# Kernel tuning notes

Measured on AMD Instinct MI355X. Metric: run time of the kernel, lower is better.

## Reference

```python
import jax, jax.numpy as jnp
import numpy as np
from jax.scipy.special import logsumexp

EPSILON = 0.05
MAX_ITER = 50
TOL = 0.001


def setup_inputs() -> dict:
    key = jax.random.key(0)
    k1, k2, k3 = jax.random.split(key, 3)
    B, N, M = 32, 1024, 1024
    cost = jax.random.uniform(k1, (B, N, M), dtype=jnp.float32)  # non-negative
    src = jax.random.uniform(k2, (B, N), dtype=jnp.float32) + 0.1
    tgt = jax.random.uniform(k3, (B, M), dtype=jnp.float32) + 0.1
    src = src / jnp.sum(src, axis=-1, keepdims=True)
    tgt = tgt / jnp.sum(tgt, axis=-1, keepdims=True)
    return {"cost": cost, "source_marginal": src, "target_marginal": tgt}


def reference(cost, source_marginal, target_marginal):
    B, N, M = cost.shape
    log_r = jnp.log(source_marginal + 1e-12)  # [B,N]
    log_c = jnp.log(target_marginal + 1e-12)  # [B,M]
    log_K = -cost / EPSILON                    # [B,N,M]

    log_u0 = jnp.zeros((B, N), dtype=cost.dtype)
    log_v0 = jnp.zeros((B, M), dtype=cost.dtype)

    def step(carry, _):
        log_u, log_v, done = carry
        # row update: logsumexp over M
        new_u = log_r - logsumexp(log_K + log_v[:, None, :], axis=-1)
        # col update: logsumexp over N (uses freshly updated u, as in torch)
        new_v = log_c - logsumexp(log_K + new_u[:, :, None], axis=-2)
        change = jnp.max(jnp.abs(new_u - log_u))  # global max, like torch
        # emulate early break: freeze state once converged
        log_u_next = jnp.where(done, log_u, new_u)
        log_v_next = jnp.where(done, log_v, new_v)
        done_next = done | (change < TOL)
        return (log_u_next, log_v_next, done_next), None

    (log_u, log_v, _), _ = jax.lax.scan(
        step, (log_u0, log_v0, jnp.array(False)), None, length=MAX_ITER
    )

    log_T = log_u[:, :, None] + log_K + log_v[:, None, :]
    return jnp.exp(log_T)
```

## Files before the change

### kernel.cpp

```cpp
#include <hip/hip_runtime.h>
#include <math.h>

#define INV_EPS  (-20.0f)
#define QINV     (1.0f / 65535.0f)
#define LN65535  11.090354888959125f
#define TOLV     0.001f
#define MAX_ITER 50
#define NBLK     256
#define NTHR     1024

#define CTRL_CNT(g)   ((g) * 64)
#define CTRL_GEN(g)   ((g) * 64 + 32)
#define CTRL_ARR(d)   (2048 + (d) * 32)
#define CTRL_CHG(d)   (3648 + (d) * 32)
#define CTRL_INTS     5248
#define Q_OFF_BYTES   (1u << 20)

#define RX __ATOMIC_RELAXED
#define SC __HIP_MEMORY_SCOPE_AGENT

__device__ __forceinline__ float wave_red_sum64(float x) {
    x += __int_as_float(__builtin_amdgcn_update_dpp(0, __float_as_int(x), 0x111, 0xf, 0xf, false));
    x += __int_as_float(__builtin_amdgcn_update_dpp(0, __float_as_int(x), 0x112, 0xf, 0xf, false));
    x += __int_as_float(__builtin_amdgcn_update_dpp(0, __float_as_int(x), 0x114, 0xf, 0xf, false));
    x += __int_as_float(__builtin_amdgcn_update_dpp(0, __float_as_int(x), 0x118, 0xf, 0xf, false));
    x += __int_as_float(__builtin_amdgcn_update_dpp(0, __float_as_int(x), 0x142, 0xf, 0xf, false));
    x += __int_as_float(__builtin_amdgcn_update_dpp(0, __float_as_int(x), 0x143, 0xf, 0xf, false));
    return __int_as_float(__builtin_amdgcn_readlane(__float_as_int(x), 63));
}

__device__ __forceinline__ void group_sync(int* cnt, int* gen) {
    __syncthreads();
    if (threadIdx.x == 0) {
        int g = __hip_atomic_load(gen, RX, SC);
        int a = __hip_atomic_fetch_add(cnt, 1, RX, SC);
        if (a == 7) {
            __hip_atomic_store(cnt, 0, RX, SC);
            __hip_atomic_store(gen, g + 1, RX, SC);
        } else {
            while (__hip_atomic_load(gen, RX, SC) == g)
                __builtin_amdgcn_s_sleep(1);
        }
    }
    __syncthreads();
}

#define ROWMATH(LR)                                                            \
  {                                                                            \
    float sA = fmaf(qf0, evs0, fmaf(qf4, evs4, fmaf(qf8,  evs8,  qf12*evs12)));\
    float sB = fmaf(qf1, evs1, fmaf(qf5, evs5, fmaf(qf9,  evs9,  qf13*evs13)));\
    float sC = fmaf(qf2, evs2, fmaf(qf6, evs6, fmaf(qf10, evs10, qf14*evs14)));\
    float sD = fmaf(qf3, evs3, fmaf(qf7, evs7, fmaf(qf11, evs11, qf15*evs15)));\
    float s = (sA + sB) + (sC + sD);                                           \
    s = wave_red_sum64(s);                                                     \
    float u_new = lg_src[LR] - __logf(s);                                      \
    flag |= (fabsf(u_new - u_ring[pv][LR]) >= TOLV);                           \
    if (lane == 0) u_ring[cur][LR] = u_new;                                    \
    float eu = __expf(u_new);                                                  \
    cs0 = fmaf(qf0, eu, cs0);   cs1 = fmaf(qf1, eu, cs1);                      \
    cs2 = fmaf(qf2, eu, cs2);   cs3 = fmaf(qf3, eu, cs3);                      \
    cs4 = fmaf(qf4, eu, cs4);   cs5 = fmaf(qf5, eu, cs5);                      \
    cs6 = fmaf(qf6, eu, cs6);   cs7 = fmaf(qf7, eu, cs7);                      \
    cs8 = fmaf(qf8, eu, cs8);   cs9 = fmaf(qf9, eu, cs9);                      \
    cs10 = fmaf(qf10, eu, cs10); cs11 = fmaf(qf11, eu, cs11);                  \
    cs12 = fmaf(qf12, eu, cs12); cs13 = fmaf(qf13, eu, cs13);                  \
    cs14 = fmaf(qf14, eu, cs14); cs15 = fmaf(qf15, eu, cs15);                  \
  }

#define ROW_LIN(QA, QB, LR)                                                    \
  {                                                                            \
    float qf0  = (float)((QA).x & 0xffffu), qf1  = (float)((QA).x >> 16),      \
          qf2  = (float)((QA).y & 0xffffu), qf3  = (float)((QA).y >> 16),      \
          qf4  = (float)((QA).z & 0xffffu), qf5  = (float)((QA).z >> 16),      \
          qf6  = (float)((QA).w & 0xffffu), qf7  = (float)((QA).w >> 16),      \
          qf8  = (float)((QB).x & 0xffffu), qf9  = (float)((QB).x >> 16),      \
          qf10 = (float)((QB).y & 0xffffu), qf11 = (float)((QB).y >> 16),      \
          qf12 = (float)((QB).z & 0xffffu), qf13 = (float)((QB).z >> 16),      \
          qf14 = (float)((QB).w & 0xffffu), qf15 = (float)((QB).w >> 16);      \
    ROWMATH(LR)                                                                \
  }

template<int QM>
__global__ __launch_bounds__(NTHR, 4) void sinkhorn_fused(
    const float* __restrict__ cost, const float* __restrict__ src,
    const float* __restrict__ tgt, float* __restrict__ out,
    int* __restrict__ ctrl, uint* __restrict__ qbuf)
{
    const int t    = threadIdx.x;
    const int lane = t & 63;
    const int widx = t >> 6;
    const int rx   = blockIdx.x & 7;
    const int sx   = blockIdx.x >> 3;
    const int grp  = rx * 4 + (sx >> 3);
    const int j    = sx & 7;

    __shared__ float smS[16][64][17];
    __shared__ float v_ring[4][1024];
    __shared__ float u_ring[4][128];
    __shared__ float lg_tgt[1024];
    __shared__ float lg_src[128];
    __shared__ int   s_chg, s_stop;

    int* cnt = ctrl + CTRL_CNT(grp);
    int* gen = ctrl + CTRL_GEN(grp);

    const int rowb = (grp << 10) + (j << 7);
    const float* cbase = cost + ((size_t)(rowb + (widx << 3)) << 10) + (lane << 2);
    uint4* qb4 = nullptr;
    if constexpr (QM == 1)
        qb4 = (uint4*)qbuf + (size_t)(rowb + (widx << 3)) * 128 + lane;
    float* const Pg = out + ((size_t)grp << 20);

    lg_tgt[t] = __logf(tgt[(grp << 10) + t] + 1e-12f) + ((QM == 1) ? LN65535 : 0.f);
    if (t < 128) {
        lg_src[t]    = __logf(src[rowb + t] + 1e-12f);
        u_ring[3][t] = 0.f;
    }
    v_ring[3][t] = 0.f;

    float4 f0, f1, f2, f3, g0, g1, g2, g3;
    if constexpr (QM == 0) {
        f0 = *(const float4*)(cbase);
        f1 = *(const float4*)(cbase + 256);
        f2 = *(const float4*)(cbase + 512);
        f3 = *(const float4*)(cbase + 768);
        const float* r1p = cbase + ((size_t)1 << 10);
        g0 = *(const float4*)(r1p);
        g1 = *(const float4*)(r1p + 256);
        g2 = *(const float4*)(r1p + 512);
        g3 = *(const float4*)(r1p + 768);
    }
    uint4 uf0 = {}, uf1 = {}, ug0 = {}, ug1 = {};

    __syncthreads();

    int K = -1;
    for (int it = 0; it < MAX_ITER; ++it) {
        const int cur = it & 3, pv = (it + 3) & 3;

        if (t == 0) {
            int stop = 0;
            if (it >= 2) {
                const int d = it - 2;
                while (__hip_atomic_load(ctrl + CTRL_ARR(d), RX, SC) != NBLK)
                    __builtin_amdgcn_s_sleep(1);
                stop = (__hip_atomic_load(ctrl + CTRL_CHG(d), RX, SC) == 0);
            }
            s_stop = stop;
            s_chg  = 0;
        }
        __syncthreads();
        if (s_stop) { K = it - 2; break; }

        bool flag = false;

        if constexpr (QM == 1) {
            const int r8 = widx << 3;
            const float* vp = &v_ring[pv][lane << 2];
            float4 va = *(const float4*)vp;
            float4 vb = *(const float4*)(vp + 256);
            float4 vc = *(const float4*)(vp + 512);
            float4 vd = *(const float4*)(vp + 768);
            const float evs0  = __expf(va.x)*QINV, evs1  = __expf(va.y)*QINV,
                        evs2  = __expf(va.z)*QINV, evs3  = __expf(va.w)*QINV,
                        evs4  = __expf(vb.x)*QINV, evs5  = __expf(vb.y)*QINV,
                        evs6  = __expf(vb.z)*QINV, evs7  = __expf(vb.w)*QINV,
                        evs8  = __expf(vc.x)*QINV, evs9  = __expf(vc.y)*QINV,
                        evs10 = __expf(vc.z)*QINV, evs11 = __expf(vc.w)*QINV,
                        evs12 = __expf(vd.x)*QINV, evs13 = __expf(vd.y)*QINV,
                        evs14 = __expf(vd.z)*QINV, evs15 = __expf(vd.w)*QINV;
            float cs0=0,cs1=0,cs2=0,cs3=0,cs4=0,cs5=0,cs6=0,cs7=0,
                  cs8=0,cs9=0,cs10=0,cs11=0,cs12=0,cs13=0,cs14=0,cs15=0;

            if (it == 0) {
                float4 a0 = *(const float4*)(cbase);
                float4 a1 = *(const float4*)(cbase + 256);
                float4 a2 = *(const float4*)(cbase + 512);
                float4 a3 = *(const float4*)(cbase + 768);
                const float* r1p = cbase + ((size_t)1 << 10);
                float4 b0 = *(const float4*)(r1p);
                float4 b1 = *(const float4*)(r1p + 256);
                float4 b2 = *(const float4*)(r1p + 512);
                float4 b3 = *(const float4*)(r1p + 768);
                #pragma unroll 1
                for (int i = 0; i < 8; ++i) {
                    const float* nxt = cbase + ((size_t)((i + 2) & 7) << 10);
                    float4 p0 = *(const float4*)(nxt);
                    float4 p1 = *(const float4*)(nxt + 256);
                    float4 p2 = *(const float4*)(nxt + 512);
                    float4 p3 = *(const float4*)(nxt + 768);

                    float qf0  = rintf(__expf(a0.x*INV_EPS)*65535.f);
                    float qf1  = rintf(__expf(a0.y*INV_EPS)*65535.f);
                    float qf2  = rintf(__expf(a0.z*INV_EPS)*65535.f);
                    float qf3  = rintf(__expf(a0.w*INV_EPS)*65535.f);
                    float qf4  = rintf(__expf(a1.x*INV_EPS)*65535.f);
                    float qf5  = rintf(__expf(a1.y*INV_EPS)*65535.f);
                    float qf6  = rintf(__expf(a1.z*INV_EPS)*65535.f);
                    float qf7  = rintf(__expf(a1.w*INV_EPS)*65535.f);
                    float qf8  = rintf(__expf(a2.x*INV_EPS)*65535.f);
                    float qf9  = rintf(__expf(a2.y*INV_EPS)*65535.f);
                    float qf10 = rintf(__expf(a2.z*INV_EPS)*65535.f);
                    float qf11 = rintf(__expf(a2.w*INV_EPS)*65535.f);
                    float qf12 = rintf(__expf(a3.x*INV_EPS)*65535.f);
                    float qf13 = rintf(__expf(a3.y*INV_EPS)*65535.f);
                    float qf14 = rintf(__expf(a3.z*INV_EPS)*65535.f);
                    float qf15 = rintf(__expf(a3.w*INV_EPS)*65535.f);
                    uint4 w0, w1;
                    w0.x = (uint)qf0  | ((uint)qf1  << 16);
                    w0.y = (uint)qf2  | ((uint)qf3  << 16);
                    w0.z = (uint)qf4  | ((uint)qf5  << 16);
                    w0.w = (uint)qf6  | ((uint)qf7  << 16);
                    w1.x = (uint)qf8  | ((uint)qf9  << 16);
                    w1.y = (uint)qf10 | ((uint)qf11 << 16);
                    w1.z = (uint)qf12 | ((uint)qf13 << 16);
                    w1.w = (uint)qf14 | ((uint)qf15 << 16);
                    qb4[(i << 7)]      = w0;
                    qb4[(i << 7) + 64] = w1;

                    ROWMATH(r8 + i)

                    a0 = b0; a1 = b1; a2 = b2; a3 = b3;
                    b0 = p0; b1 = p1; b2 = p2; b3 = p3;
                }
            } else {
                #pragma unroll 1
                for (int i = 0; i < 8; ++i) {
                    const int nx = ((i + 2) & 7) << 7;
                    uint4 up0 = qb4[nx];
                    uint4 up1 = qb4[nx + 64];
                    ROW_LIN(uf0, uf1, r8 + i)
                    uf0 = ug0; uf1 = ug1; ug0 = up0; ug1 = up1;
                }
            }

            smS[widx][lane][0]  = cs0;  smS[widx][lane][1]  = cs1;
            smS[widx][lane][2]  = cs2;  smS[widx][lane][3]  = cs3;
            smS[widx][lane][4]  = cs4;  smS[widx][lane][5]  = cs5;
            smS[widx][lane][6]  = cs6;  smS[widx][lane][7]  = cs7;
            smS[widx][lane][8]  = cs8;  smS[widx][lane][9]  = cs9;
            smS[widx][lane][10] = cs10; smS[widx][lane][11] = cs11;
            smS[widx][lane][12] = cs12; smS[widx][lane][13] = cs13;
            smS[widx][lane][14] = cs14; smS[widx][lane][15] = cs15;
        } else {
            const float* vp = &v_ring[pv][lane << 2];
            float4 vo0 = *(const float4*)(vp);
            float4 vo1 = *(const float4*)(vp + 256);
            float4 vo2 = *(const float4*)(vp + 512);
            float4 vo3 = *(const float4*)(vp + 768);
            float cs[16];
            #pragma unroll
            for (int s = 0; s < 16; ++s) cs[s] = 0.f;
            #pragma unroll 1
            for (int i = 0; i < 8; ++i) {
                const float* nxt = cbase + ((size_t)((i + 2) & 7) << 10);
                float4 p0 = *(const float4*)(nxt);
                float4 p1 = *(const float4*)(nxt + 256);
                float4 p2 = *(const float4*)(nxt + 512);
                float4 p3 = *(const float4*)(nxt + 768);
                float e[16];
                e[ 0] = __expf(fmaf(f0.x, INV_EPS, vo0.x));
                e[ 1] = __expf(fmaf(f0.y, INV_EPS, vo0.y));
                e[ 2] = __expf(fmaf(f0.z, INV_EPS, vo0.z));
                e[ 3] = __expf(fmaf(f0.w, INV_EPS, vo0.w));
                e[ 4] = __expf(fmaf(f1.x, INV_EPS, vo1.x));
                e[ 5] = __expf(fmaf(f1.y, INV_EPS, vo1.y));
                e[ 6] = __expf(fmaf(f1.z, INV_EPS, vo1.z));
                e[ 7] = __expf(fmaf(f1.w, INV_EPS, vo1.w));
                e[ 8] = __expf(fmaf(f2.x, INV_EPS, vo2.x));
                e[ 9] = __expf(fmaf(f2.y, INV_EPS, vo2.y));
                e[10] = __expf(fmaf(f2.z, INV_EPS, vo2.z));
                e[11] = __expf(fmaf(f2.w, INV_EPS, vo2.w));
                e[12] = __expf(fmaf(f3.x, INV_EPS, vo3.x));
                e[13] = __expf(fmaf(f3.y, INV_EPS, vo3.y));
                e[14] = __expf(fmaf(f3.z, INV_EPS, vo3.z));
                e[15] = __expf(fmaf(f3.w, INV_EPS, vo3.w));
                float s01 = e[0]+e[1],   s23 = e[2]+e[3];
                float s45 = e[4]+e[5],   s67 = e[6]+e[7];
                float s89 = e[8]+e[9],   sab = e[10]+e[11];
                float scd = e[12]+e[13], sef = e[14]+e[15];
                float s = ((s01+s23)+(s45+s67)) + ((s89+sab)+(scd+sef));
                s = wave_red_sum64(s);
                const int lr = (widx << 3) + i;
                float u_new = lg_src[lr] - __logf(s);
                flag |= (fabsf(u_new - u_ring[pv][lr]) >= TOLV);
                if (lane == 0) u_ring[cur][lr] = u_new;
                float eu = __expf(u_new);
                #pragma unroll
                for (int k = 0; k < 16; ++k)
                    cs[k] = fmaf(e[k], eu, cs[k]);
                f0 = g0; f1 = g1; f2 = g2; f3 = g3;
                g0 = p0; g1 = p1; g2 = p2; g3 = p3;
            }
            #pragma unroll
            for (int s = 0; s < 16; ++s) smS[widx][lane][s] = cs[s];
        }

        if (lane == 0 && flag) s_chg = 1;
        __syncthreads();

        if (QM == 1 && it == 0) {
            uf0 = qb4[0];   uf1 = qb4[64];
            ug0 = qb4[128]; ug1 = qb4[192];
        }

        if (t == 0) {
            if (s_chg)
                __hip_atomic_fetch_or(ctrl + CTRL_CHG(it), 1, RX, SC);
            asm volatile("s_waitcnt vmcnt(0)" ::: "memory");
            __hip_atomic_fetch_add(ctrl + CTRL_ARR(it), 1, RX, SC);
        }

        float* Pb = Pg + (size_t)(((it & 1) << 3) + j) * 1040;
        {
            const int L  = (t >> 2) & 63;
            const int sl = ((t >> 8) << 2) | (t & 3);
            float S = 0.f;
            #pragma unroll
            for (int w = 0; w < 16; ++w) S += smS[w][L][sl];
            if constexpr (QM == 0) S *= __expf(-v_ring[pv][t]);
            __hip_atomic_store(Pb + t, S, RX, SC);
        }

        group_sync(cnt, gen);

        {
            float* Pf = Pg + (size_t)((it & 1) << 3) * 1040;
            float S = 0.f;
            #pragma unroll
            for (int jj = 0; jj < 8; ++jj)
                S += __hip_atomic_load(Pf + jj * 1040 + t, RX, SC);
            v_ring[cur][t] = lg_tgt[t] - __logf(S);
        }
        __syncthreads();
    }

    if (K < 0) {
        if (t == 0) {
            while (__hip_atomic_load(ctrl + CTRL_ARR(48), RX, SC) != NBLK)
                __builtin_amdgcn_s_sleep(1);
            s_stop = (__hip_atomic_load(ctrl + CTRL_CHG(48), RX, SC) == 0);
        }
        __syncthreads();
        K = s_stop ? 48 : 49;
    }

    group_sync(cnt, gen);

    {
        const int slot = K & 3;
        const size_t base = ((size_t)rowb) << 10;
        if constexpr (QM == 1) {
            lg_tgt[t] = __expf(v_ring[slot][t]) * QINV;
            __syncthreads();
            const uint2* q2 = (const uint2*)qbuf;
            #pragma unroll 1
            for (int i = 0; i < 32; ++i) {
                const int g4  = (i << 10) + t;
                const int lr  = g4 >> 8;
                const int m0  = (g4 & 255) << 2;
                const int c   = m0 >> 8;
                const int ln  = (m0 >> 2) & 63;
                const size_t u4i = (size_t)(((rowb + lr) << 1) + (c >> 1)) * 64 + ln;
                uint2 w = q2[(u4i << 1) + (c & 1)];
                float4 ev4 = *(const float4*)&lg_tgt[m0];
                const float uu = __expf(u_ring[slot][lr]);
                float4 o;
                o.x = (float)(w.x & 0xffffu) * (uu * ev4.x);
                o.y = (float)(w.x >> 16)     * (uu * ev4.y);
                o.z = (float)(w.y & 0xffffu) * (uu * ev4.z);
                o.w = (float)(w.y >> 16)     * (uu * ev4.w);
                *(float4*)(out + base + ((size_t)g4 << 2)) = o;
            }
        } else {
            #pragma unroll 1
            for (int i = 0; i < 32; ++i) {
                const int g4  = (i << 10) + t;
                const int lr  = g4 >> 8;
                const int c4  = (g4 & 255) << 2;
                const size_t e = base + ((size_t)g4 << 2);
                float4 cc = *(const float4*)(cost + e);
                float4 vv = *(const float4*)&v_ring[slot][c4];
                const float uu = u_ring[slot][lr];
                float4 o;
                o.x = __expf(fmaf(cc.x, INV_EPS, uu + vv.x));
                o.y = __expf(fmaf(cc.y, INV_EPS, uu + vv.y));
                o.z = __expf(fmaf(cc.z, INV_EPS, uu + vv.z));
                o.w = __expf(fmaf(cc.w, INV_EPS, uu + vv.w));
                *(float4*)(out + e) = o;
            }
        }
    }
}

extern "C" void kernel_launch(void* const* d_in, const int* in_sizes, int n_in,
                              void* d_out, int out_size, void* d_ws, size_t ws_size,
                              hipStream_t stream) {
    const float* cost = (const float*)d_in[0];
    const float* src  = (const float*)d_in[1];
    const float* tgt  = (const float*)d_in[2];
    float* out = (float*)d_out;
    int*   ctrl = (int*)d_ws;
    (void)in_sizes; (void)n_in; (void)out_size;

    hipMemsetAsync(d_ws, 0, CTRL_INTS * sizeof(int), stream);

    const size_t need = (size_t)Q_OFF_BYTES + ((size_t)64 << 20);
    if (ws_size >= need) {
        uint* qbuf = (uint*)((char*)d_ws + Q_OFF_BYTES);
        sinkhorn_fused<1><<<dim3(NBLK), dim3(NTHR), 0, stream>>>(
            cost, src, tgt, out, ctrl, qbuf);
    } else {
        sinkhorn_fused<0><<<dim3(NBLK), dim3(NTHR), 0, stream>>>(
            cost, src, tgt, out, ctrl, nullptr);
    }
}
```

Baseline: 309.6 us.

## Stash half of quantized kernel in LDS and use LDS atomics for column sums

```diff
diff --git a/kernel.cpp b/kernel.cpp
--- a/kernel.cpp
+++ b/kernel.cpp
@@ -80,6 +80,48 @@
     ROWMATH(LR)                                                                \
   }
 
+#define COL_ATOMIC                                                             \
+  { const int lb = (lane << 2) + (lane >> 2);                                  \
+    atomicAdd(&colAcc[lb      ], cs0);  atomicAdd(&colAcc[lb +   1], cs1);     \
+    atomicAdd(&colAcc[lb +   2], cs2);  atomicAdd(&colAcc[lb +   3], cs3);     \
+    atomicAdd(&colAcc[lb + 272], cs4);  atomicAdd(&colAcc[lb + 273], cs5);     \
+    atomicAdd(&colAcc[lb + 274], cs6);  atomicAdd(&colAcc[lb + 275], cs7);     \
+    atomicAdd(&colAcc[lb + 544], cs8);  atomicAdd(&colAcc[lb + 545], cs9);     \
+    atomicAdd(&colAcc[lb + 546], cs10); atomicAdd(&colAcc[lb + 547], cs11);    \
+    atomicAdd(&colAcc[lb + 816], cs12); atomicAdd(&colAcc[lb + 817], cs13);    \
+    atomicAdd(&colAcc[lb + 818], cs14); atomicAdd(&colAcc[lb + 819], cs15); }
+
+#define LQS(r, p) (((((widx << 2) | (r)) << 1) | (p)) * 64 + lane)
+
+#define EPI_ROW(QA, QB, i)                                                     \
+  { const float uu = __expf(u_ring[slot][(widx << 3) + (i)]);                  \
+    float* op = out + (((size_t)(rowb + (widx << 3) + (i))) << 10) + (lane << 2); \
+    float4 ev, o;                                                              \
+    ev = *(const float4*)&lg_tgt[lane << 2];                                   \
+    o.x = (float)((QA).x & 0xffffu) * (uu * ev.x);                             \
+    o.y = (float)((QA).x >> 16)     * (uu * ev.y);                             \
+    o.z = (float)((QA).y & 0xffffu) * (uu * ev.z);                             \
+    o.w = (float)((QA).y >> 16)     * (uu * ev.w);                             \
+    *(float4*)(op) = o;                                                        \
+    ev = *(const float4*)&lg_tgt[256 + (lane << 2)];                           \
+    o.x = (float)((QA).z & 0xffffu) * (uu * ev.x);                             \
+    o.y = (float)((QA).z >> 16)     * (uu * ev.y);                             \
+    o.z = (float)((QA).w & 0xffffu) * (uu * ev.z);                             \
+    o.w = (float)((QA).w >> 16)     * (uu * ev.w);                             \
+    *(float4*)(op + 256) = o;                                                  \
+    ev = *(const float4*)&lg_tgt[512 + (lane << 2)];                           \
+    o.x = (float)((QB).x & 0xffffu) * (uu * ev.x);                             \
+    o.y = (float)((QB).x >> 16)     * (uu * ev.y);                             \
+    o.z = (float)((QB).y & 0xffffu) * (uu * ev.z);                             \
+    o.w = (float)((QB).y >> 16)     * (uu * ev.w);                             \
+    *(float4*)(op + 512) = o;                                                  \
+    ev = *(const float4*)&lg_tgt[768 + (lane << 2)];                           \
+    o.x = (float)((QB).z & 0xffffu) * (uu * ev.x);                             \
+    o.y = (float)((QB).z >> 16)     * (uu * ev.y);                             \
+    o.z = (float)((QB).w & 0xffffu) * (uu * ev.z);                             \
+    o.w = (float)((QB).w >> 16)     * (uu * ev.w);                             \
+    *(float4*)(op + 768) = o; }
+
 template<int QM>
 __global__ __launch_bounds__(NTHR, 4) void sinkhorn_fused(
     const float* __restrict__ cost, const float* __restrict__ src,
@@ -94,11 +136,12 @@
     const int grp  = rx * 4 + (sx >> 3);
     const int j    = sx & 7;
 
-    __shared__ float smS[16][64][17];
+    __shared__ float colAcc[1088];
     __shared__ float v_ring[4][1024];
     __shared__ float u_ring[4][128];
     __shared__ float lg_tgt[1024];
     __shared__ float lg_src[128];
+    __shared__ uint4 qstash[QM == 1 ? 8192 : 1];
     __shared__ int   s_chg, s_stop;
 
     int* cnt = ctrl + CTRL_CNT(grp);
@@ -106,9 +149,9 @@
 
     const int rowb = (grp << 10) + (j << 7);
     const float* cbase = cost + ((size_t)(rowb + (widx << 3)) << 10) + (lane << 2);
-    uint4* qb4 = nullptr;
+    uint4* qs4 = nullptr;
     if constexpr (QM == 1)
-        qb4 = (uint4*)qbuf + (size_t)(rowb + (widx << 3)) * 128 + lane;
+        qs4 = (uint4*)qbuf + ((size_t)((rowb >> 3) + widx)) * 512 + lane;
     float* const Pg = out + ((size_t)grp << 20);
 
     lg_tgt[t] = __logf(tgt[(grp << 10) + t] + 1e-12f) + ((QM == 1) ? LN65535 : 0.f);
@@ -130,13 +173,15 @@
         g2 = *(const float4*)(r1p + 512);
         g3 = *(const float4*)(r1p + 768);
     }
-    uint4 uf0 = {}, uf1 = {}, ug0 = {}, ug1 = {};
 
     __syncthreads();
 
     int K = -1;
     for (int it = 0; it < MAX_ITER; ++it) {
         const int cur = it & 3, pv = (it + 3) & 3;
+
+        colAcc[t] = 0.f;
+        if (t < 64) colAcc[1024 + t] = 0.f;
 
         if (t == 0) {
             int stop = 0;
@@ -215,8 +260,13 @@
                     w1.y = (uint)qf10 | ((uint)qf11 << 16);
                     w1.z = (uint)qf12 | ((uint)qf13 << 16);
                     w1.w = (uint)qf14 | ((uint)qf15 << 16);
-                    qb4[(i << 7)]      = w0;
-                    qb4[(i << 7) + 64] = w1;
+                    if (i < 4) {
+                        qstash[LQS(i, 0)] = w0;
+                        qstash[LQS(i, 1)] = w1;
+                    } else {
+                        qs4[((i - 4) << 7)]      = w0;
+                        qs4[((i - 4) << 7) + 64] = w1;
+                    }
 
                     ROWMATH(r8 + i)
 
@@ -224,24 +274,21 @@
                     b0 = p0; b1 = p1; b2 = p2; b3 = p3;
                 }
             } else {
-                #pragma unroll 1
-                for (int i = 0; i < 8; ++i) {
-                    const int nx = ((i + 2) & 7) << 7;
-                    uint4 up0 = qb4[nx];
-                    uint4 up1 = qb4[nx + 64];
-                    ROW_LIN(uf0, uf1, r8 + i)
-                    uf0 = ug0; uf1 = ug1; ug0 = up0; ug1 = up1;
-                }
+                uint4 p40 = qs4[0],   p41 = qs4[64];
+                uint4 p50 = qs4[128], p51 = qs4[192];
+                uint4 p60 = qs4[256], p61 = qs4[320];
+                uint4 p70 = qs4[384], p71 = qs4[448];
+                { uint4 l0 = qstash[LQS(0,0)], l1 = qstash[LQS(0,1)]; ROW_LIN(l0, l1, r8+0) }
+                { uint4 l0 = qstash[LQS(1,0)], l1 = qstash[LQS(1,1)]; ROW_LIN(l0, l1, r8+1) }
+                { uint4 l0 = qstash[LQS(2,0)], l1 = qstash[LQS(2,1)]; ROW_LIN(l0, l1, r8+2) }
+                { uint4 l0 = qstash[LQS(3,0)], l1 = qstash[LQS(3,1)]; ROW_LIN(l0, l1, r8+3) }
+                ROW_LIN(p40, p41, r8+4)
+                ROW_LIN(p50, p51, r8+5)
+                ROW_LIN(p60, p61, r8+6)
+                ROW_LIN(p70, p71, r8+7)
             }
 
-            smS[widx][lane][0]  = cs0;  smS[widx][lane][1]  = cs1;
-            smS[widx][lane][2]  = cs2;  smS[widx][lane][3]  = cs3;
-            smS[widx][lane][4]  = cs4;  smS[widx][lane][5]  = cs5;
-            smS[widx][lane][6]  = cs6;  smS[widx][lane][7]  = cs7;
-            smS[widx][lane][8]  = cs8;  smS[widx][lane][9]  = cs9;
-            smS[widx][lane][10] = cs10; smS[widx][lane][11] = cs11;
-            smS[widx][lane][12] = cs12; smS[widx][lane][13] = cs13;
-            smS[widx][lane][14] = cs14; smS[widx][lane][15] = cs15;
+            COL_ATOMIC
         } else {
             const float* vp = &v_ring[pv][lane << 2];
             float4 vo0 = *(const float4*)(vp);
@@ -292,17 +339,14 @@
                 f0 = g0; f1 = g1; f2 = g2; f3 = g3;
                 g0 = p0; g1 = p1; g2 = p2; g3 = p3;
             }
+            const int lb = (lane << 2) + (lane >> 2);
             #pragma unroll
-            for (int s = 0; s < 16; ++s) smS[widx][lane][s] = cs[s];
+            for (int k = 0; k < 16; ++k)
+                atomicAdd(&colAcc[(k >> 2) * 272 + lb + (k & 3)], cs[k]);
         }
 
         if (lane == 0 && flag) s_chg = 1;
         __syncthreads();
-
-        if (QM == 1 && it == 0) {
-            uf0 = qb4[0];   uf1 = qb4[64];
-            ug0 = qb4[128]; ug1 = qb4[192];
-        }
 
         if (t == 0) {
             if (s_chg)
@@ -313,11 +357,7 @@
 
         float* Pb = Pg + (size_t)(((it & 1) << 3) + j) * 1040;
         {
-            const int L  = (t >> 2) & 63;
-            const int sl = ((t >> 8) << 2) | (t & 3);
-            float S = 0.f;
-            #pragma unroll
-            for (int w = 0; w < 16; ++w) S += smS[w][L][sl];
+            float S = colAcc[t + (t >> 4)];
             if constexpr (QM == 0) S *= __expf(-v_ring[pv][t]);
             __hip_atomic_store(Pb + t, S, RX, SC);
         }
@@ -349,30 +389,23 @@
 
     {
         const int slot = K & 3;
-        const size_t base = ((size_t)rowb) << 10;
         if constexpr (QM == 1) {
+            uint4 p40 = qs4[0],   p41 = qs4[64];
+            uint4 p50 = qs4[128], p51 = qs4[192];
+            uint4 p60 = qs4[256], p61 = qs4[320];
+            uint4 p70 = qs4[384], p71 = qs4[448];
             lg_tgt[t] = __expf(v_ring[slot][t]) * QINV;
             __syncthreads();
-            const uint2* q2 = (const uint2*)qbuf;
-            #pragma unroll 1
-            for (int i = 0; i < 32; ++i) {
-                const int g4  = (i << 10) + t;
-                const int lr  = g4 >> 8;
-                const int m0  = (g4 & 255) << 2;
-                const int c   = m0 >> 8;
-                const int ln  = (m0 >> 2) & 63;
-                const size_t u4i = (size_t)(((rowb + lr) << 1) + (c >> 1)) * 64 + ln;
-                uint2 w = q2[(u4i << 1) + (c & 1)];
-                float4 ev4 = *(const float4*)&lg_tgt[m0];
-                const float uu = __expf(u_ring[slot][lr]);
-                float4 o;
-                o.x = (float)(w.x & 0xffffu) * (uu * ev4.x);
-                o.y = (float)(w.x >> 16)     * (uu * ev4.y);
-                o.z = (float)(w.y & 0xffffu) * (uu * ev4.z);
-                o.w = (float)(w.y >> 16)     * (uu * ev4.w);
-                *(float4*)(out + base + ((size_t)g4 << 2)) = o;
-            }
+            { uint4 l0 = qstash[LQS(0,0)], l1 = qstash[LQS(0,1)]; EPI_ROW(l0, l1, 0) }
+            { uint4 l0 = qstash[LQS(1,0)], l1 = qstash[LQS(1,1)]; EPI_ROW(l0, l1, 1) }
+            { uint4 l0 = qstash[LQS(2,0)], l1 = qstash[LQS(2,1)]; EPI_ROW(l0, l1, 2) }
+            { uint4 l0 = qstash[LQS(3,0)], l1 = qstash[LQS(3,1)]; EPI_ROW(l0, l1, 3) }
+            EPI_ROW(p40, p41, 4)
+            EPI_ROW(p50, p51, 5)
+            EPI_ROW(p60, p61, 6)
+            EPI_ROW(p70, p71, 7)
         } else {
+            const size_t base = ((size_t)rowb) << 10;
             #pragma unroll 1
             for (int i = 0; i < 32; ++i) {
                 const int g4  = (i << 10) + t;
@@ -405,7 +438,7 @@
 
     hipMemsetAsync(d_ws, 0, CTRL_INTS * sizeof(int), stream);
 
-    const size_t need = (size_t)Q_OFF_BYTES + ((size_t)64 << 20);
+    const size_t need = (size_t)Q_OFF_BYTES + ((size_t)32 << 20);
     if (ws_size >= need) {
         uint* qbuf = (uint*)((char*)d_ws + Q_OFF_BYTES);
         sinkhorn_fused<1><<<dim3(NBLK), dim3(NTHR), 0, stream>>>(
```

Result: slower. 445.4 us (+43.9%).
